# Performance work log

Measured on AMD Instinct MI355X. Metric: run time of the kernel, lower is better.

## Reference

```python
import jax, jax.numpy as jnp
import numpy as np

N, D, K = 131072, 768, 2000


def setup_inputs() -> dict:
    key = jax.random.key(0)
    kx, kc = jax.random.split(key)
    x = jax.random.normal(kx, (N, D), dtype=jnp.float32)
    centroids = jax.random.normal(kc, (D, K), dtype=jnp.float32)  # stored as [D, K] like the torch module
    return {"x": x, "centroids": centroids}


def reference(x, centroids):
    # dist[n,k] = ||x_n||^2 - 2 x_n . c_k + ||c_k||^2  (matmul trick)
    x_norm = jnp.sum(x * x, axis=1, keepdims=True)              # [N, 1]
    c_norm = jnp.sum(centroids * centroids, axis=0, keepdims=True)  # [1, K]
    dist = x_norm - 2.0 * jnp.matmul(x, centroids) + c_norm     # [N, K]
    return jnp.argmin(dist, axis=-1)                            # [N] int
```

## Files before the change

### kernel.cpp

```cpp
#include <hip/hip_runtime.h>
#include <hip/hip_bf16.h>

#define N_ROWS 131072
#define DIM    768
#define K_C    2000
#define K_PAD  2048
#define TAU    0.2f
#define LISTCAP 8192

typedef _Float16 f16;
typedef _Float16 f16x4 __attribute__((ext_vector_type(4)));
typedef _Float16 f16x8 __attribute__((ext_vector_type(8)));
typedef float    f32x4 __attribute__((ext_vector_type(4)));

#define OFF_CN   6291456
#define OFF_XN   6299648
#define OFF_PMIN 6823936
#define OFF_PSEC 15212544
#define OFF_PIDX 23601152
#define OFF_CNT  31989760
#define OFF_LIST 31990016
#define OFF_CN64 32022784
#define OFF_XH   32039168

static __device__ __forceinline__ void gload16(const void* g, void* l) {
  __builtin_amdgcn_global_load_lds(
      (const __attribute__((address_space(1))) unsigned int*)g,
      (__attribute__((address_space(3))) unsigned int*)l, 16, 0, 0);
}

__global__ void prep_cn(const float* __restrict__ cent, float* __restrict__ cn,
                        double* __restrict__ cn64) {
#pragma clang fp contract(off)
  int k = blockIdx.x * 256 + threadIdx.x;
  float s = 0.0f;
  double s64 = 0.0;
  for (int d = 0; d < DIM; ++d) {
    float c = (k < K_C) ? cent[d * K_C + k] : 0.0f;
    float sq = c * c;
    s = s + sq;
    s64 += (double)c * (double)c;
  }
  cn[k] = (k < K_C) ? s : INFINITY;
  cn64[k] = (k < K_C) ? s64 : (double)INFINITY;
}

__global__ __launch_bounds__(256) void prep_ct(const float* __restrict__ cent,
                                               f16* __restrict__ cTh) {
  __shared__ float ld[64][65];
  int k0 = blockIdx.x * 64;
  int d0 = blockIdx.y * 64;
  int tid = threadIdx.x;
#pragma unroll
  for (int it = 0; it < 16; ++it) {
    int idx = it * 256 + tid;
    int dd = idx >> 6, kk = idx & 63;
    int k = k0 + kk;
    ld[dd][kk] = (k < K_C) ? cent[(size_t)(d0 + dd) * K_C + k] : 0.0f;
  }
  __syncthreads();
#pragma unroll
  for (int it = 0; it < 16; ++it) {
    int idx = it * 256 + tid;
    int kk = idx >> 6, dd = idx & 63;
    cTh[(size_t)(k0 + kk) * DIM + d0 + dd] = (f16)ld[dd][kk];
  }
}

__global__ __launch_bounds__(256) void xnorm_prepx(const float* __restrict__ x,
                                                   float* __restrict__ xn,
                                                   f16* __restrict__ xh) {
#pragma clang fp contract(off)
  __shared__ __align__(16) float buf[16 * DIM];
  int row0 = blockIdx.x * 16;
  int tid = threadIdx.x;
  const f32x4* src = (const f32x4*)(x + (size_t)row0 * DIM);
  f32x4* dst = (f32x4*)buf;
#pragma unroll
  for (int c = 0; c < 12; ++c) {
    f32x4 v = src[c * 256 + tid];
    dst[c * 256 + tid] = v;
    f16x4 hv;
#pragma unroll
    for (int j = 0; j < 4; ++j) hv[j] = (f16)v[j];
    *(f16x4*)(xh + (size_t)row0 * DIM + (size_t)(c * 256 + tid) * 4) = hv;
  }
  __syncthreads();
  int w = tid >> 6, lane = tid & 63;
  int b = lane >> 3, j = lane & 7;
#pragma unroll
  for (int rr = 0; rr < 4; ++rr) {
    int r = w * 4 + rr;
    const float* a = buf + r * DIM + 96 * b + j;
    float v0 = a[0];
    float acc = v0 * v0;
#pragma unroll
    for (int t = 1; t < 12; ++t) {
      float q = a[8 * t];
      float s = q * q;
      acc = acc + s;
    }
    float v = acc;
    { float o = __shfl_xor(v, 1);  v = v + o; }
    { float o = __shfl_xor(v, 2);  v = v + o; }
    { float o = __shfl_xor(v, 4);  v = v + o; }
    { float o = __shfl_xor(v, 8);  v = v + o; }
    { float o = __shfl_xor(v, 16); v = v + o; }
    { float o = __shfl_xor(v, 32); v = v + o; }
    if (lane == 0) xn[row0 + r] = v;
  }
}

#define STAGE(bufb, ktv)                                                       \
  do {                                                                         \
    _Pragma("unroll") for (int i_ = 0; i_ < 4; ++i_) {                         \
      int q_ = w * 4 + i_;                                                     \
      int s0_ = q_ * 1024 + lane * 16;                                         \
      int row_ = s0_ >> 7;                                                     \
      int sl_ = ((s0_ >> 4) & 7) ^ (row_ & 7);                                 \
      size_t ga_ = (size_t)(rb * 128 + row_) * DIM + (ktv) * 64 + sl_ * 8;     \
      size_t gb_ = (size_t)(pb * 128 + row_) * DIM + (ktv) * 64 + sl_ * 8;     \
      gload16(xh + ga_, ldsb + (bufb) + q_ * 1024);                            \
      gload16(cTh + gb_, ldsb + 32768 + (bufb) + q_ * 1024);                   \
    }                                                                          \
  } while (0)

__global__ __launch_bounds__(256, 2) void kmeans_main(
    const f16* __restrict__ xh, const f16* __restrict__ cTh,
    const float* __restrict__ cn, const float* __restrict__ xn,
    float* __restrict__ pmin, float* __restrict__ psec,
    int* __restrict__ pidx) {
  __shared__ __align__(16) f16 lds[32768];
  char* ldsb = (char*)lds;

  int d0 = blockIdx.x;
  int g  = (d0 & 7) * 2048 + (d0 >> 3);
  int pb = g & 15;
  int rb = g >> 4;

  int tid  = threadIdx.x;
  int w    = tid >> 6;
  int lane = tid & 63;
  int wrow = (w >> 1) * 64;
  int wcol = (w & 1) * 64;

  int rsel = lane & 15;
  int ksel = lane >> 4;
  int rs0 = ((ksel ^ (rsel & 7))) << 4;
  int rs1 = (((4 + ksel) ^ (rsel & 7))) << 4;

  f32x4 acc[4][4] = {};

  STAGE(0, 0);
  STAGE(16384, 1);

  for (int kt = 0; kt < 12; ++kt) {
    int bufb = (kt & 1) * 16384;
    if (kt < 11) {
      asm volatile("s_waitcnt vmcnt(8)" ::: "memory");
    } else {
      asm volatile("s_waitcnt vmcnt(0)" ::: "memory");
    }
    __builtin_amdgcn_sched_barrier(0);
    __builtin_amdgcn_s_barrier();
    __builtin_amdgcn_sched_barrier(0);

    f16x8 ah[2][4], bh[2][4];
#pragma unroll
    for (int m = 0; m < 4; ++m) {
      int rbase = bufb + (wrow + m * 16 + rsel) * 128;
      ah[0][m] = *(const f16x8*)(ldsb + rbase + rs0);
      ah[1][m] = *(const f16x8*)(ldsb + rbase + rs1);
    }
#pragma unroll
    for (int n = 0; n < 4; ++n) {
      int rbase = bufb + 32768 + (wcol + n * 16 + rsel) * 128;
      bh[0][n] = *(const f16x8*)(ldsb + rbase + rs0);
      bh[1][n] = *(const f16x8*)(ldsb + rbase + rs1);
    }
    __builtin_amdgcn_sched_barrier(0);
    asm volatile("s_waitcnt lgkmcnt(0)" ::: "memory");
    __builtin_amdgcn_sched_barrier(0);
    __builtin_amdgcn_s_barrier();
    __builtin_amdgcn_sched_barrier(0);

    if (kt < 10) STAGE(bufb, kt + 2);

    __builtin_amdgcn_s_setprio(1);
#pragma unroll
    for (int k32 = 0; k32 < 2; ++k32)
#pragma unroll
      for (int m = 0; m < 4; ++m)
#pragma unroll
        for (int n = 0; n < 4; ++n)
          acc[m][n] = __builtin_amdgcn_mfma_f32_16x16x32_f16(
              ah[k32][m], bh[k32][n], acc[m][n], 0, 0, 0);
    __builtin_amdgcn_s_setprio(0);
  }

  __syncthreads();
  float* lv = (float*)lds;
  float* lsv = (float*)lds + 256;
  int*   li = (int*)((float*)lds + 512);

  int colbase = pb * 128 + wcol + rsel;
  float cnv[4];
#pragma unroll
  for (int n = 0; n < 4; ++n) cnv[n] = cn[colbase + n * 16];
  int g4 = ksel * 4;

#pragma unroll
  for (int m = 0; m < 4; ++m) {
#pragma unroll
    for (int j = 0; j < 4; ++j) {
      int trow = wrow + m * 16 + g4 + j;
      float xv = xn[rb * 128 + trow];
      float v1 = 0.0f, v2 = INFINITY;
      int i1 = 0;
#pragma unroll
      for (int n = 0; n < 4; ++n) {
        float dd = (xv - 2.0f * acc[m][n][j]) + cnv[n];
        int ci = colbase + n * 16;
        if (n == 0) { v1 = dd; i1 = ci; }
        else if (dd < v1) { v2 = v1; v1 = dd; i1 = ci; }
        else { v2 = fminf(v2, dd); }
      }
#pragma unroll
      for (int off = 1; off < 16; off <<= 1) {
        float ov1 = __shfl_xor(v1, off);
        float ov2 = __shfl_xor(v2, off);
        int oi1 = __shfl_xor(i1, off);
        if (ov1 < v1 || (ov1 == v1 && oi1 < i1)) {
          v2 = fminf(v1, ov2); v1 = ov1; i1 = oi1;
        } else {
          v2 = fminf(v2, ov1);
        }
      }
      if ((lane & 15) == 0) {
        lv[(w & 1) * 128 + trow] = v1;
        lsv[(w & 1) * 128 + trow] = v2;
        li[(w & 1) * 128 + trow] = i1;
      }
    }
  }
  __syncthreads();
  if (tid < 128) {
    float a1 = lv[tid], a2 = lsv[tid];
    int aj = li[tid];
    float b1 = lv[128 + tid], b2 = lsv[128 + tid];
    int bj = li[128 + tid];
    float v1, v2; int i1;
    if (b1 < a1 || (b1 == a1 && bj < aj)) { v1 = b1; i1 = bj; v2 = fminf(b2, a1); }
    else { v1 = a1; i1 = aj; v2 = fminf(a2, b1); }
    size_t o = (size_t)pb * N_ROWS + rb * 128 + tid;
    pmin[o] = v1;
    psec[o] = v2;
    pidx[o] = i1;
  }
}

__global__ void merge_detect(const float* __restrict__ pmin,
                             const float* __restrict__ psec,
                             const int* __restrict__ pidx, int* __restrict__ out,
                             int* __restrict__ list, int* __restrict__ counter) {
  int n = blockIdx.x * 256 + threadIdx.x;
  float v1 = INFINITY, v2 = INFINITY;
  int i1 = 0x7fffffff;
  for (int p = 0; p < 16; ++p) {
    float a1 = pmin[(size_t)p * N_ROWS + n];
    float a2 = psec[(size_t)p * N_ROWS + n];
    int aj = pidx[(size_t)p * N_ROWS + n];
    if (a1 < v1 || (a1 == v1 && aj < i1)) {
      v2 = fminf(v1, a2); v1 = a1; i1 = aj;
    } else {
      v2 = fminf(v2, a1);
    }
  }
  out[n] = i1;
  if (v2 - v1 < TAU) {
    int idx = atomicAdd(counter, 1);
    if (idx < LISTCAP) list[idx] = n;
  }
}

__global__ __launch_bounds__(256) void exact_recheck64(
    const float* __restrict__ x, const float* __restrict__ cent,
    const double* __restrict__ cn64, const int* __restrict__ list,
    const int* __restrict__ counter, int* __restrict__ out) {
  __shared__ __align__(16) float xrow[DIM];
  __shared__ double rv[256];
  __shared__ int ri[256];
  int b = blockIdx.x;
  if (b >= counter[0]) return;
  int n = list[b];
  int tid = threadIdx.x;
  double part = 0.0;
  for (int d = tid; d < DIM; d += 256) {
    float v = x[(size_t)n * DIM + d];
    xrow[d] = v;
    part += (double)v * (double)v;
  }
  rv[tid] = part;
  __syncthreads();
  for (int s = 128; s > 0; s >>= 1) {
    if (tid < s) rv[tid] += rv[tid + s];
    __syncthreads();
  }
  double xn64 = rv[0];
  __syncthreads();

  int k7 = tid + 1792;
  int k7c = (k7 < K_C) ? k7 : (K_C - 1);
  double a0 = 0, a1 = 0, a2 = 0, a3 = 0, a4 = 0, a5 = 0, a6 = 0, a7 = 0;
#pragma unroll 4
  for (int d = 0; d < DIM; ++d) {
    double xv = (double)xrow[d];
    const float* cp = cent + (size_t)d * K_C + tid;
    a0 = fma(xv, (double)cp[0], a0);
    a1 = fma(xv, (double)cp[256], a1);
    a2 = fma(xv, (double)cp[512], a2);
    a3 = fma(xv, (double)cp[768], a3);
    a4 = fma(xv, (double)cp[1024], a4);
    a5 = fma(xv, (double)cp[1280], a5);
    a6 = fma(xv, (double)cp[1536], a6);
    a7 = fma(xv, (double)(cp[k7c - tid]), a7);
  }

  double bv = (double)INFINITY;
  int bi = 0x7fffffff;
  double dots[8] = {a0, a1, a2, a3, a4, a5, a6, a7};
#pragma unroll
  for (int j = 0; j < 8; ++j) {
    int k = tid + j * 256;
    if (k < K_C) {
      double dd = (xn64 - 2.0 * dots[j]) + cn64[k];
      if (dd < bv) { bv = dd; bi = k; }
    }
  }
  rv[tid] = bv;
  ri[tid] = bi;
  __syncthreads();
  for (int s = 128; s > 0; s >>= 1) {
    if (tid < s) {
      double ov = rv[tid + s];
      int oi = ri[tid + s];
      if (ov < rv[tid] || (ov == rv[tid] && oi < ri[tid])) {
        rv[tid] = ov; ri[tid] = oi;
      }
    }
    __syncthreads();
  }
  if (tid == 0) out[n] = ri[0];
}

extern "C" void kernel_launch(void* const* d_in, const int* in_sizes, int n_in,
                              void* d_out, int out_size, void* d_ws, size_t ws_size,
                              hipStream_t stream) {
  const float* x = (const float*)d_in[0];
  const float* cent = (const float*)d_in[1];
  char* ws = (char*)d_ws;
  f16* cTh = (f16*)ws;
  float* cn = (float*)(ws + OFF_CN);
  float* xn = (float*)(ws + OFF_XN);
  float* pmin = (float*)(ws + OFF_PMIN);
  float* psec = (float*)(ws + OFF_PSEC);
  int* pidx = (int*)(ws + OFF_PIDX);
  int* counter = (int*)(ws + OFF_CNT);
  int* list = (int*)(ws + OFF_LIST);
  double* cn64 = (double*)(ws + OFF_CN64);
  f16* xh = (f16*)(ws + OFF_XH);

  hipMemsetAsync(counter, 0, 4, stream);
  prep_cn<<<8, 256, 0, stream>>>(cent, cn, cn64);
  prep_ct<<<dim3(32, 12), 256, 0, stream>>>(cent, cTh);
  xnorm_prepx<<<N_ROWS / 16, 256, 0, stream>>>(x, xn, xh);
  kmeans_main<<<16384, 256, 0, stream>>>(xh, cTh, cn, xn, pmin, psec, pidx);
  merge_detect<<<N_ROWS / 256, 256, 0, stream>>>(pmin, psec, pidx, (int*)d_out,
                                                 list, counter);
  exact_recheck64<<<LISTCAP, 256, 0, stream>>>(x, cent, cn64, list, counter,
                                               (int*)d_out);
}
```

Before: 1.260 ms.

## Load A operand directly from global and batch exact recheck four rows per block

The main GEMM kernel no longer stages x tiles through LDS. Each wave reads its A fragments straight from global memory, which halves LDS use and lets launch bounds rise to three blocks per CU. The intent is to cut LDS traffic and barrier pressure and to raise occupancy, at the cost of uncoalesced, unshared global reads of x across the two waves that use the same rows. The exact double-precision recheck now handles four candidate rows per block, so each centroid load is reused four times, at the cost of more registers per thread.

```diff
diff --git a/kernel.cpp b/kernel.cpp
--- a/kernel.cpp
+++ b/kernel.cpp
@@ -111,26 +111,24 @@
   }
 }
 
-#define STAGE(bufb, ktv)                                                       \
+#define STAGE_B(bufb, ktv)                                                     \
   do {                                                                         \
     _Pragma("unroll") for (int i_ = 0; i_ < 4; ++i_) {                         \
       int q_ = w * 4 + i_;                                                     \
       int s0_ = q_ * 1024 + lane * 16;                                         \
       int row_ = s0_ >> 7;                                                     \
       int sl_ = ((s0_ >> 4) & 7) ^ (row_ & 7);                                 \
-      size_t ga_ = (size_t)(rb * 128 + row_) * DIM + (ktv) * 64 + sl_ * 8;     \
       size_t gb_ = (size_t)(pb * 128 + row_) * DIM + (ktv) * 64 + sl_ * 8;     \
-      gload16(xh + ga_, ldsb + (bufb) + q_ * 1024);                            \
-      gload16(cTh + gb_, ldsb + 32768 + (bufb) + q_ * 1024);                   \
+      gload16(cTh + gb_, ldsb + (bufb) + q_ * 1024);                           \
     }                                                                          \
   } while (0)
 
-__global__ __launch_bounds__(256, 2) void kmeans_main(
+__global__ __launch_bounds__(256, 3) void kmeans_main(
     const f16* __restrict__ xh, const f16* __restrict__ cTh,
     const float* __restrict__ cn, const float* __restrict__ xn,
     float* __restrict__ pmin, float* __restrict__ psec,
     int* __restrict__ pidx) {
-  __shared__ __align__(16) f16 lds[32768];
+  __shared__ __align__(16) f16 lds[16384];
   char* ldsb = (char*)lds;
 
   int d0 = blockIdx.x;
@@ -149,15 +147,18 @@
   int rs0 = ((ksel ^ (rsel & 7))) << 4;
   int rs1 = (((4 + ksel) ^ (rsel & 7))) << 4;
 
+  const char* aptr = (const char*)xh +
+      ((size_t)(rb * 128 + wrow + rsel) * DIM + (size_t)ksel * 8) * 2;
+
   f32x4 acc[4][4] = {};
 
-  STAGE(0, 0);
-  STAGE(16384, 1);
+  STAGE_B(0, 0);
+  STAGE_B(16384, 1);
 
   for (int kt = 0; kt < 12; ++kt) {
     int bufb = (kt & 1) * 16384;
     if (kt < 11) {
-      asm volatile("s_waitcnt vmcnt(8)" ::: "memory");
+      asm volatile("s_waitcnt vmcnt(4)" ::: "memory");
     } else {
       asm volatile("s_waitcnt vmcnt(0)" ::: "memory");
     }
@@ -168,13 +169,13 @@
     f16x8 ah[2][4], bh[2][4];
 #pragma unroll
     for (int m = 0; m < 4; ++m) {
-      int rbase = bufb + (wrow + m * 16 + rsel) * 128;
-      ah[0][m] = *(const f16x8*)(ldsb + rbase + rs0);
-      ah[1][m] = *(const f16x8*)(ldsb + rbase + rs1);
+      const char* ab = aptr + m * 24576;
+      ah[0][m] = *(const f16x8*)(ab);
+      ah[1][m] = *(const f16x8*)(ab + 64);
     }
 #pragma unroll
     for (int n = 0; n < 4; ++n) {
-      int rbase = bufb + 32768 + (wcol + n * 16 + rsel) * 128;
+      int rbase = bufb + (wcol + n * 16 + rsel) * 128;
       bh[0][n] = *(const f16x8*)(ldsb + rbase + rs0);
       bh[1][n] = *(const f16x8*)(ldsb + rbase + rs1);
     }
@@ -184,7 +185,7 @@
     __builtin_amdgcn_s_barrier();
     __builtin_amdgcn_sched_barrier(0);
 
-    if (kt < 10) STAGE(bufb, kt + 2);
+    if (kt < 10) STAGE_B(bufb, kt + 2);
 
     __builtin_amdgcn_s_setprio(1);
 #pragma unroll
@@ -196,6 +197,8 @@
           acc[m][n] = __builtin_amdgcn_mfma_f32_16x16x32_f16(
               ah[k32][m], bh[k32][n], acc[m][n], 0, 0, 0);
     __builtin_amdgcn_s_setprio(0);
+
+    aptr += 128;
   }
 
   __syncthreads();
@@ -283,74 +286,90 @@
   }
 }
 
+#define ACCS(R) \
+  double a##R##0 = 0, a##R##1 = 0, a##R##2 = 0, a##R##3 = 0, \
+         a##R##4 = 0, a##R##5 = 0, a##R##6 = 0, a##R##7 = 0
+#define FMAS(R, XV) \
+  a##R##0 = fma(XV, c0, a##R##0); a##R##1 = fma(XV, c1, a##R##1); \
+  a##R##2 = fma(XV, c2, a##R##2); a##R##3 = fma(XV, c3, a##R##3); \
+  a##R##4 = fma(XV, c4, a##R##4); a##R##5 = fma(XV, c5, a##R##5); \
+  a##R##6 = fma(XV, c6, a##R##6); a##R##7 = fma(XV, c7, a##R##7)
+#define EVAL(R)                                                         \
+  {                                                                     \
+    double dots[8] = {a##R##0, a##R##1, a##R##2, a##R##3,               \
+                      a##R##4, a##R##5, a##R##6, a##R##7};              \
+    double bv = (double)INFINITY;                                       \
+    int bi = 0x7fffffff;                                                \
+    _Pragma("unroll") for (int j = 0; j < 8; ++j) {                     \
+      int k = tid + j * 256;                                            \
+      if (k < K_C) {                                                    \
+        double dd = (xnorms[R] - 2.0 * dots[j]) + cn64[k];              \
+        if (dd < bv) { bv = dd; bi = k; }                               \
+      }                                                                 \
+    }                                                                   \
+    rv[tid] = bv; ri[tid] = bi;                                         \
+    __syncthreads();                                                    \
+    for (int s = 128; s > 0; s >>= 1) {                                 \
+      if (tid < s) {                                                    \
+        double ov = rv[tid + s];                                        \
+        int oi = ri[tid + s];                                           \
+        if (ov < rv[tid] || (ov == rv[tid] && oi < ri[tid])) {          \
+          rv[tid] = ov; ri[tid] = oi;                                   \
+        }                                                               \
+      }                                                                 \
+      __syncthreads();                                                  \
+    }                                                                   \
+    if (tid == 0 && (R) < nrows) out[list[b0 + (R)]] = ri[0];           \
+    __syncthreads();                                                    \
+  }
+
 __global__ __launch_bounds__(256) void exact_recheck64(
     const float* __restrict__ x, const float* __restrict__ cent,
     const double* __restrict__ cn64, const int* __restrict__ list,
     const int* __restrict__ counter, int* __restrict__ out) {
-  __shared__ __align__(16) float xrow[DIM];
+  __shared__ __align__(16) float xrow[4][DIM];
   __shared__ double rv[256];
   __shared__ int ri[256];
-  int b = blockIdx.x;
-  if (b >= counter[0]) return;
-  int n = list[b];
+  __shared__ double xnorms[4];
+  int cnt = counter[0];
+  if (cnt > LISTCAP) cnt = LISTCAP;
+  int b0 = blockIdx.x * 4;
+  if (b0 >= cnt) return;
+  int nrows = cnt - b0;
+  if (nrows > 4) nrows = 4;
   int tid = threadIdx.x;
-  double part = 0.0;
-  for (int d = tid; d < DIM; d += 256) {
-    float v = x[(size_t)n * DIM + d];
-    xrow[d] = v;
-    part += (double)v * (double)v;
-  }
-  rv[tid] = part;
-  __syncthreads();
-  for (int s = 128; s > 0; s >>= 1) {
-    if (tid < s) rv[tid] += rv[tid + s];
+  for (int r = 0; r < 4; ++r) {
+    int n = list[b0 + (r < nrows ? r : 0)];
+    double part = 0.0;
+    for (int d = tid; d < DIM; d += 256) {
+      float v = x[(size_t)n * DIM + d];
+      xrow[r][d] = v;
+      part += (double)v * (double)v;
+    }
+    rv[tid] = part;
     __syncthreads();
-  }
-  double xn64 = rv[0];
-  __syncthreads();
+    for (int s = 128; s > 0; s >>= 1) {
+      if (tid < s) rv[tid] += rv[tid + s];
+      __syncthreads();
+    }
+    if (tid == 0) xnorms[r] = rv[0];
+    __syncthreads();
+  }
 
   int k7 = tid + 1792;
   int k7c = (k7 < K_C) ? k7 : (K_C - 1);
-  double a0 = 0, a1 = 0, a2 = 0, a3 = 0, a4 = 0, a5 = 0, a6 = 0, a7 = 0;
-#pragma unroll 4
+  ACCS(0); ACCS(1); ACCS(2); ACCS(3);
+#pragma unroll 2
   for (int d = 0; d < DIM; ++d) {
-    double xv = (double)xrow[d];
     const float* cp = cent + (size_t)d * K_C + tid;
-    a0 = fma(xv, (double)cp[0], a0);
-    a1 = fma(xv, (double)cp[256], a1);
-    a2 = fma(xv, (double)cp[512], a2);
-    a3 = fma(xv, (double)cp[768], a3);
-    a4 = fma(xv, (double)cp[1024], a4);
-    a5 = fma(xv, (double)cp[1280], a5);
-    a6 = fma(xv, (double)cp[1536], a6);
-    a7 = fma(xv, (double)(cp[k7c - tid]), a7);
-  }
-
-  double bv = (double)INFINITY;
-  int bi = 0x7fffffff;
-  double dots[8] = {a0, a1, a2, a3, a4, a5, a6, a7};
-#pragma unroll
-  for (int j = 0; j < 8; ++j) {
-    int k = tid + j * 256;
-    if (k < K_C) {
-      double dd = (xn64 - 2.0 * dots[j]) + cn64[k];
-      if (dd < bv) { bv = dd; bi = k; }
-    }
-  }
-  rv[tid] = bv;
-  ri[tid] = bi;
-  __syncthreads();
-  for (int s = 128; s > 0; s >>= 1) {
-    if (tid < s) {
-      double ov = rv[tid + s];
-      int oi = ri[tid + s];
-      if (ov < rv[tid] || (ov == rv[tid] && oi < ri[tid])) {
-        rv[tid] = ov; ri[tid] = oi;
-      }
-    }
-    __syncthreads();
-  }
-  if (tid == 0) out[n] = ri[0];
+    double c0 = cp[0], c1 = cp[256], c2 = cp[512], c3 = cp[768];
+    double c4 = cp[1024], c5 = cp[1280], c6 = cp[1536];
+    double c7 = cp[k7c - tid];
+    double x0 = xrow[0][d], x1 = xrow[1][d];
+    double x2 = xrow[2][d], x3 = xrow[3][d];
+    FMAS(0, x0); FMAS(1, x1); FMAS(2, x2); FMAS(3, x3);
+  }
+  EVAL(0) EVAL(1) EVAL(2) EVAL(3)
 }
 
 extern "C" void kernel_launch(void* const* d_in, const int* in_sizes, int n_in,
@@ -377,6 +396,6 @@
   kmeans_main<<<16384, 256, 0, stream>>>(xh, cTh, cn, xn, pmin, psec, pidx);
   merge_detect<<<N_ROWS / 256, 256, 0, stream>>>(pmin, psec, pidx, (int*)d_out,
                                                  list, counter);
-  exact_recheck64<<<LISTCAP, 256, 0, stream>>>(x, cent, cn64, list, counter,
-                                               (int*)d_out);
-}
+  exact_recheck64<<<LISTCAP / 4, 256, 0, stream>>>(x, cent, cn64, list, counter,
+                                                   (int*)d_out);
+}
```

Measured after the change: 1.597 ms. 26.7% more time.
